# Kernel tuning notes

Hardware: AMD Instinct MI355X
Metric: run time of the kernel (lower is better)

## Reference

```python
import jax
import jax.numpy as jnp
import numpy as np

# Config mirroring GLOBAL_CONFIG['attn'] / kernel config in the source
BM = 64            # query-group (block) size; asserted 64 or 192 in source
TOP_KEYS = 0.1     # fraction of keys kept via top-k on colsum scores
MULTIPLE_OF = 64   # counts_multiple_of: indices_count rounded to this
LW1D = 0.15        # local_1d_window fraction
RAND_INV_PROB = 100

B, H, N, D = 1, 12, 2048, 128


def setup_inputs() -> dict:
    key = jax.random.key(0)
    kq, kk, kv, kc = jax.random.split(key, 4)
    shape = (B, H, N, D)
    q = jax.random.normal(kq, shape, dtype=jnp.float32)
    k = jax.random.normal(kk, shape, dtype=jnp.float32)
    v = jax.random.normal(kv, shape, dtype=jnp.float32)
    out_cache = jax.random.normal(kc, shape, dtype=jnp.float32)
    return {"q": q, "k": k, "v": v, "out_cache": out_cache}


def _static_1d_mask(n: int, bm: int, lw1d: float) -> jnp.ndarray:
    # initialize_1d_static_mask: per query-group local window centered at
    # qg*bm + bm//2, width int(lw1d*n), clipped to [0, n). Shape [qg, n].
    qg = n // bm
    ws = int(lw1d * n)
    centers = jnp.arange(qg) * bm + bm // 2          # [qg]
    j = jnp.arange(n)                                  # [n]
    lo = centers[:, None] - ws // 2
    hi = centers[:, None] + ws // 2
    return (j[None, :] >= lo) & (j[None, :] < hi)


def _scatter_true(mask, idx):
    # mask.scatter_(-1, idx, True) along last axis
    K = idx.shape[-1]
    n = mask.shape[-1]
    flat = mask.reshape(-1, n)
    fidx = idx.reshape(-1, K)
    rows = jnp.arange(flat.shape[0])[:, None]
    flat = flat.at[rows, fidx].set(True)
    return flat.reshape(mask.shape)


def _sparse_diff_attn(q, k, v, out_cache):
    b, h, n, d = q.shape
    qg = n // BM
    scale = 1.0 / jnp.sqrt(jnp.asarray(d, q.dtype))
    # dense scores (dense_colsum_attn computes these on the full step)
    scores = jnp.einsum('bhid,bhjd->bhij', q, k) * scale   # [b,h,n,n]
    probs = jax.nn.softmax(scores, axis=-1)
    # bs: column-sum of attention probabilities per query group  [b,h,qg,n]
    bs = probs.reshape(b, h, qg, BM, n).sum(axis=3)
    # indices_count = multiple_of * round(top_keys * n / multiple_of)
    indices_count = MULTIPLE_OF * int(round(TOP_KEYS * n / MULTIPLE_OF))
    rmask = jax.random.randint(jax.random.key(1), bs.shape, 0, RAND_INV_PROB) == 0
    _, idx = jax.lax.top_k(bs, indices_count)
    mask = _scatter_true(rmask, idx)                       # [b,h,qg,n]
    static = _static_1d_mask(n, BM, LW1D)                  # [qg,n]
    # video_query_groups: groups where static window + topk still sparse
    vqg = (static.sum(axis=-1, keepdims=True) + indices_count) < n  # [qg,1]
    mask = mask & vqg[None, None]
    mask = mask | static[None, None]
    # csp_attn: block-sparse attention; every query i in group i//BM attends
    # only to keys selected in mask[.., i//BM, :]
    full_mask = jnp.repeat(mask, BM, axis=2)               # [b,h,n,n]
    sp_scores = jnp.where(full_mask, scores, -jnp.inf)
    sp_probs = jax.nn.softmax(sp_scores, axis=-1)
    sp_out = jnp.einsum('bhij,bhjd->bhid', sp_probs, v)
    # sparse step: o = o_cache + csp_attn(...)  (sign = +1)
    return out_cache + sp_out


def reference(q, k, v, out_cache):
    return _sparse_diff_attn(q, k, v, out_cache)
```

## Files before the change

### kernel.cpp

```cpp
#include <hip/hip_runtime.h>
#include <math.h>

constexpr int Hh   = 12;
constexpr int Nn   = 2048;
constexpr int Dd   = 128;
constexpr int BMq  = 64;
constexpr int QGg  = 32;
constexpr int KSEL = 192;
constexpr int CK   = 32;
constexpr float SCALE = 0.08838834764831845f;

typedef _Float16 v8h __attribute__((ext_vector_type(8)));
typedef float    v4f __attribute__((ext_vector_type(4)));

__device__ __attribute__((aligned(16))) _Float16 g_qh[(size_t)Hh*Nn*Dd];
__device__ __attribute__((aligned(16))) _Float16 g_ql[(size_t)Hh*Nn*Dd];
__device__ __attribute__((aligned(16))) _Float16 g_kh[(size_t)Hh*Nn*Dd];
__device__ __attribute__((aligned(16))) _Float16 g_kl[(size_t)Hh*Nn*Dd];
__device__ float          g_lp[(size_t)Hh*Nn*16];
__device__ float          g_bs[(size_t)Hh*QGg*Nn];
__device__ unsigned short g_sel[Hh*QGg*Nn];
__device__ int            g_cnt[Hh*QGg];

__device__ __forceinline__ unsigned int rotl32(unsigned int x, int n){
  return (x << n) | (x >> (32 - n));
}

__device__ __forceinline__ unsigned pack2h(_Float16 a, _Float16 b){
  unsigned short ua, ub;
  __builtin_memcpy(&ua, &a, 2);
  __builtin_memcpy(&ub, &b, 2);
  return (unsigned)ua | ((unsigned)ub << 16);
}

__device__ __forceinline__ void tf2x32(unsigned int k0, unsigned int k1,
                                       unsigned int x0, unsigned int x1,
                                       unsigned int &o0, unsigned int &o1){
  const unsigned int ks2 = 0x1BD11BDAu ^ k0 ^ k1;
  x0 += k0; x1 += k1;
  x0 += x1; x1 = rotl32(x1,13); x1 ^= x0;
  x0 += x1; x1 = rotl32(x1,15); x1 ^= x0;
  x0 += x1; x1 = rotl32(x1,26); x1 ^= x0;
  x0 += x1; x1 = rotl32(x1, 6); x1 ^= x0;
  x0 += k1; x1 += ks2 + 1u;
  x0 += x1; x1 = rotl32(x1,17); x1 ^= x0;
  x0 += x1; x1 = rotl32(x1,29); x1 ^= x0;
  x0 += x1; x1 = rotl32(x1,16); x1 ^= x0;
  x0 += x1; x1 = rotl32(x1,24); x1 ^= x0;
  x0 += ks2; x1 += k0 + 2u;
  x0 += x1; x1 = rotl32(x1,13); x1 ^= x0;
  x0 += x1; x1 = rotl32(x1,15); x1 ^= x0;
  x0 += x1; x1 = rotl32(x1,26); x1 ^= x0;
  x0 += x1; x1 = rotl32(x1, 6); x1 ^= x0;
  x0 += k0; x1 += k1 + 3u;
  x0 += x1; x1 = rotl32(x1,17); x1 ^= x0;
  x0 += x1; x1 = rotl32(x1,29); x1 ^= x0;
  x0 += x1; x1 = rotl32(x1,16); x1 ^= x0;
  x0 += x1; x1 = rotl32(x1,24); x1 ^= x0;
  x0 += k1; x1 += ks2 + 4u;
  x0 += x1; x1 = rotl32(x1,13); x1 ^= x0;
  x0 += x1; x1 = rotl32(x1,15); x1 ^= x0;
  x0 += x1; x1 = rotl32(x1,26); x1 ^= x0;
  x0 += x1; x1 = rotl32(x1, 6); x1 ^= x0;
  x0 += ks2; x1 += k0 + 5u;
  o0 = x0; o1 = x1;
}

__device__ __forceinline__ bool jax_rand01(unsigned int idx,
                                           unsigned int k1a, unsigned int k1b,
                                           unsigned int k2a, unsigned int k2b){
  unsigned int h0, h1, l0, l1;
  tf2x32(k1a, k1b, 0u, idx, h0, h1);
  tf2x32(k2a, k2b, 0u, idx, l0, l1);
  unsigned int h = h0 ^ h1;
  unsigned int l = l0 ^ l1;
  unsigned int off = ((h % 100u) * 96u + (l % 100u)) % 100u;
  return off == 0u;
}

__global__ __launch_bounds__(256) void k0_cvt(const float* __restrict__ Q,
                                              const float* __restrict__ K){
  const int bid = blockIdx.x;
  const int t = threadIdx.x;
  const int kc = t >> 6, ln = t & 63;
  const int row = ln & 15;
  const int col = kc*32 + (ln >> 4)*8;
  const size_t src = ((size_t)bid*16 + row)*Dd + col;
  const size_t ob  = (((size_t)bid)*4 + kc)*512 + (size_t)ln*8;

  float4 qa = *(const float4*)(Q + src);
  float4 qb = *(const float4*)(Q + src + 4);
  float qs[8] = {qa.x*SCALE, qa.y*SCALE, qa.z*SCALE, qa.w*SCALE,
                 qb.x*SCALE, qb.y*SCALE, qb.z*SCALE, qb.w*SCALE};
  v8h qh, ql;
  #pragma unroll
  for (int j = 0; j < 8; ++j){
    _Float16 hi = (_Float16)qs[j];
    qh[j] = hi;
    ql[j] = (_Float16)(qs[j] - (float)hi);
  }
  *(v8h*)&g_qh[ob] = qh;
  *(v8h*)&g_ql[ob] = ql;

  float4 ka = *(const float4*)(K + src);
  float4 kb = *(const float4*)(K + src + 4);
  float ks[8] = {ka.x, ka.y, ka.z, ka.w, kb.x, kb.y, kb.z, kb.w};
  v8h kh, kl;
  #pragma unroll
  for (int j = 0; j < 8; ++j){
    _Float16 hi = (_Float16)ks[j];
    kh[j] = hi;
    kl[j] = (_Float16)(ks[j] - (float)hi);
  }
  *(v8h*)&g_kh[ob] = kh;
  *(v8h*)&g_kl[ob] = kl;
}

__global__ __launch_bounds__(256) void k1_rowsum(){
  const int bid0 = blockIdx.x;
  const int w = (bid0 & 7)*384 + (bid0 >> 3);
  const int jb = w & 15, gp = (w >> 4) & 15, h = w >> 8;
  const int t = threadIdx.x;
  const int wv = t >> 6, ln = t & 63;
  const int nidx = ln & 15, quad = ln >> 4;
  const size_t lnoff = (size_t)ln*8;
  const size_t habase = ((size_t)h*128 + gp*8 + wv*2)*4;
  const size_t hbbase = ((size_t)h*128 + jb*8)*4;

  v4f acc[2][8];
  #pragma unroll
  for (int tr = 0; tr < 2; ++tr)
    #pragma unroll
    for (int tc = 0; tc < 8; ++tc)
      acc[tr][tc] = (v4f){0.f, 0.f, 0.f, 0.f};

  for (int kc = 0; kc < 4; ++kc){
    v8h ahi[2], alo[2];
    #pragma unroll
    for (int tr = 0; tr < 2; ++tr){
      const size_t ab = (habase + tr*4 + kc)*512 + lnoff;
      ahi[tr] = *(const v8h*)&g_qh[ab];
      alo[tr] = *(const v8h*)&g_ql[ab];
    }
    v8h bhi[8], blo[8];
    #pragma unroll
    for (int tc = 0; tc < 8; ++tc){
      const size_t bb = (hbbase + tc*4 + kc)*512 + lnoff;
      bhi[tc] = *(const v8h*)&g_kh[bb];
      blo[tc] = *(const v8h*)&g_kl[bb];
    }
    #pragma unroll
    for (int tr = 0; tr < 2; ++tr)
      #pragma unroll
      for (int tc = 0; tc < 8; ++tc){
        acc[tr][tc] = __builtin_amdgcn_mfma_f32_16x16x32_f16(ahi[tr], bhi[tc], acc[tr][tc], 0, 0, 0);
        acc[tr][tc] = __builtin_amdgcn_mfma_f32_16x16x32_f16(ahi[tr], blo[tc], acc[tr][tc], 0, 0, 0);
        acc[tr][tc] = __builtin_amdgcn_mfma_f32_16x16x32_f16(alo[tr], bhi[tc], acc[tr][tc], 0, 0, 0);
      }
  }

  #pragma unroll
  for (int tr = 0; tr < 2; ++tr){
    float rs[4] = {0.f, 0.f, 0.f, 0.f};
    #pragma unroll
    for (int tc = 0; tc < 8; ++tc){
      #pragma unroll
      for (int r = 0; r < 4; ++r){
        rs[r] += __expf(acc[tr][tc][r]);
      }
    }
    #pragma unroll
    for (int r = 0; r < 4; ++r){
      float v = rs[r];
      v += __shfl_xor(v, 1);
      v += __shfl_xor(v, 2);
      v += __shfl_xor(v, 4);
      v += __shfl_xor(v, 8);
      rs[r] = v;
    }
    if (nidx == 0){
      #pragma unroll
      for (int r = 0; r < 4; ++r){
        const int row = (wv*2+tr)*16 + quad*4 + r;
        g_lp[((size_t)h*Nn + gp*128 + row)*16 + jb] = rs[r];
      }
    }
  }
}

__global__ __launch_bounds__(256) void k2r_colsum(){
  const int bid0 = blockIdx.x;
  const int w = (bid0 & 7)*384 + (bid0 >> 3);
  const int jb = w & 15, gp = (w >> 4) & 15, h = w >> 8;
  const int t = threadIdx.x;
  const int wv = t >> 6, ln = t & 63;
  const int nidx = ln & 15, quad = ln >> 4;
  const size_t lnoff = (size_t)ln*8;
  const size_t habase = ((size_t)h*128 + gp*8 + wv*2)*4;
  const size_t hbbase = ((size_t)h*128 + jb*8)*4;

  __shared__ float il_s[128];
  __shared__ float part[4][128];
  if (t < 128){
    const float* lp = &g_lp[((size_t)h*Nn + gp*128 + t)*16];
    float s = 0.f;
    #pragma unroll
    for (int x = 0; x < 16; ++x) s += lp[x];
    il_s[t] = 1.0f / s;
  }
  __syncthreads();

  v4f acc[2][8];
  #pragma unroll
  for (int tr = 0; tr < 2; ++tr)
    #pragma unroll
    for (int tc = 0; tc < 8; ++tc)
      acc[tr][tc] = (v4f){0.f, 0.f, 0.f, 0.f};

  for (int kc = 0; kc < 4; ++kc){
    v8h ahi[2], alo[2];
    #pragma unroll
    for (int tr = 0; tr < 2; ++tr){
      const size_t ab = (habase + tr*4 + kc)*512 + lnoff;
      ahi[tr] = *(const v8h*)&g_qh[ab];
      alo[tr] = *(const v8h*)&g_ql[ab];
    }
    v8h bhi[8], blo[8];
    #pragma unroll
    for (int tc = 0; tc < 8; ++tc){
      const size_t bb = (hbbase + tc*4 + kc)*512 + lnoff;
      bhi[tc] = *(const v8h*)&g_kh[bb];
      blo[tc] = *(const v8h*)&g_kl[bb];
    }
    #pragma unroll
    for (int tr = 0; tr < 2; ++tr)
      #pragma unroll
      for (int tc = 0; tc < 8; ++tc){
        acc[tr][tc] = __builtin_amdgcn_mfma_f32_16x16x32_f16(ahi[tr], bhi[tc], acc[tr][tc], 0, 0, 0);
        acc[tr][tc] = __builtin_amdgcn_mfma_f32_16x16x32_f16(ahi[tr], blo[tc], acc[tr][tc], 0, 0, 0);
        acc[tr][tc] = __builtin_amdgcn_mfma_f32_16x16x32_f16(alo[tr], bhi[tc], acc[tr][tc], 0, 0, 0);
      }
  }

  float csg[8];
  #pragma unroll
  for (int tc = 0; tc < 8; ++tc) csg[tc] = 0.f;
  #pragma unroll
  for (int tr = 0; tr < 2; ++tr){
    #pragma unroll
    for (int tc = 0; tc < 8; ++tc){
      float cs = 0.f;
      #pragma unroll
      for (int r = 0; r < 4; ++r){
        const int row = (wv*2+tr)*16 + quad*4 + r;
        cs += __expf(acc[tr][tc][r]) * il_s[row];
      }
      cs += __shfl_xor(cs, 16);
      cs += __shfl_xor(cs, 32);
      csg[tc] += cs;
    }
  }
  if (ln < 16){
    #pragma unroll
    for (int tc = 0; tc < 8; ++tc) part[wv][tc*16 + nidx] = csg[tc];
  }
  __syncthreads();
  const int col = t & 127, grp = t >> 7;
  g_bs[((size_t)h*QGg + gp*2 + grp)*Nn + jb*128 + col] =
      part[grp*2][col] + part[grp*2 + 1][col];
}

__global__ __launch_bounds__(256) void k2b_mask(){
  const int bid = blockIdx.x, g = bid % QGg, t = threadIdx.x;
  const int wv = t >> 6, lw = t & 63;
  __shared__ int hist[256];
  __shared__ int wsum[4];
  __shared__ int selb_s, selgt_s;
  __shared__ int csel;
  __shared__ int eqn;
  __shared__ int eqpos[Nn];
  const float* src = g_bs + (size_t)bid*Nn;
  float mine[8];
  {
    float4 a = *(const float4*)&src[t*4];
    float4 b = *(const float4*)&src[1024 + t*4];
    mine[0]=a.x; mine[1]=a.y; mine[2]=a.z; mine[3]=a.w;
    mine[4]=b.x; mine[5]=b.y; mine[6]=b.z; mine[7]=b.w;
  }
  if (t == 0){ csel = 0; eqn = 0; }
  unsigned int bu8[8];
  #pragma unroll
  for (int u = 0; u < 8; ++u) bu8[u] = __float_as_uint(mine[u]);

  unsigned int k1a, k1b, k2a, k2b;
  tf2x32(0u, 1u, 0u, 0u, k1a, k1b);
  tf2x32(0u, 1u, 0u, 1u, k2a, k2b);

  unsigned int pref = 0u;
  unsigned int msk  = 0u;
  int rem = KSEL;
  #pragma unroll
  for (int pass = 3; pass >= 0; --pass){
    const int shift = pass*8;
    hist[t] = 0;
    __syncthreads();
    #pragma unroll
    for (int u = 0; u < 8; ++u){
      if ((bu8[u] & msk) == pref)
        atomicAdd(&hist[(bu8[u] >> shift) & 0xFFu], 1);
    }
    __syncthreads();
    const int hcnt = hist[t];
    int s = hcnt;
    #pragma unroll
    for (int d = 1; d < 64; d <<= 1){
      int tmp = __shfl_down(s, d);
      if (lw + d < 64) s += tmp;
    }
    if (lw == 0) wsum[wv] = s;
    __syncthreads();
    int base = 0;
    #pragma unroll
    for (int w2 = 1; w2 < 4; ++w2) if (wv + w2 < 4) base += wsum[wv + w2];
    const int gt_incl = s + base;
    const int gt = gt_incl - hcnt;
    if (gt < rem && gt_incl >= rem){ selb_s = t; selgt_s = gt; }
    __syncthreads();
    pref |= ((unsigned)selb_s) << shift;
    msk  |= 0xFFu << shift;
    rem  -= selgt_s;
  }
  const unsigned int T = pref;
  const int need = rem;

  #pragma unroll
  for (int u = 0; u < 8; ++u){
    int j = (u < 4) ? (t*4 + u) : (1024 + t*4 + u - 4);
    if (bu8[u] == T){
      int s = atomicAdd(&eqn, 1);
      eqpos[s] = j;
    }
  }
  __syncthreads();
  const int en = eqn;

  const int lo = g*BMq + BMq/2 - 153;
  const int hi = g*BMq + BMq/2 + 153;
  const int ssum = ((hi < Nn) ? hi : Nn) - ((lo > 0) ? lo : 0);
  const bool vqg = (ssum + KSEL) < Nn;

  #pragma unroll
  for (int u = 0; u < 8; ++u){
    int j = (u < 4) ? (t*4 + u) : (1024 + t*4 + u - 4);
    unsigned int bu = bu8[u];
    bool topk = bu > T;
    if (!topk && bu == T){
      int tr = 0;
      for (int i = 0; i < en; ++i)
        tr += (eqpos[i] < j) ? 1 : 0;
      topk = (tr < need);
    }
    bool rnd = jax_rand01((unsigned)(bid*Nn + j), k1a, k1b, k2a, k2b);
    bool st  = (j >= lo) && (j < hi);
    bool selb = st || ((rnd || topk) && vqg);
    if (selb){
      int slot = atomicAdd(&csel, 1);
      g_sel[(size_t)bid*Nn + slot] = (unsigned short)j;
    }
  }
  __syncthreads();
  if (t == 0) g_cnt[bid] = csel;
}

__global__ __launch_bounds__(256) void k3_attn(const float* __restrict__ K,
                                               const float* __restrict__ V,
                                               const float* __restrict__ OC,
                                               float* __restrict__ out){
  const int bid0 = blockIdx.x;
  const int w    = (bid0 & 7)*96 + (bid0 >> 3);
  const int half = w & 1;
  const int gg   = w >> 1;
  const int h = gg / QGg, g = gg % QGg;
  const int t = threadIdx.x;
  const int wv = t >> 6, ln = t & 63;
  const int nidx = ln & 15, quad = ln >> 4;
  const int qtile = wv >> 1, kdt = wv & 1;

  __shared__ _Float16 kh_s[CK][136];
  __shared__ _Float16 kl_s[CK][136];
  __shared__ float    vT[Dd][33];
  __shared__ _Float16 p_h[32][40];
  __shared__ _Float16 p_l[32][40];
  __shared__ float    l_part[2][32];
  __shared__ float    l_s[32];

  const int c = g_cnt[gg];
  const unsigned short* sel = g_sel + (size_t)gg*Nn;

  const int rb = g*4 + half*2 + qtile;
  v8h aHi[4], aLo[4];
  #pragma unroll
  for (int kc = 0; kc < 4; ++kc){
    const size_t ab = (((size_t)h*128 + rb)*4 + kc)*512 + (size_t)ln*8;
    aHi[kc] = *(const v8h*)&g_qh[ab];
    aLo[kc] = *(const v8h*)&g_ql[ab];
  }

  if (t < 64) l_part[t >> 5][t & 31] = 0.0f;
  __syncthreads();

  v4f acc[4];
  #pragma unroll
  for (int dt = 0; dt < 4; ++dt) acc[dt] = (v4f){0.f, 0.f, 0.f, 0.f};

  for (int c0 = 0; c0 < c; c0 += CK){
    const int cc = ((c - c0) < CK) ? (c - c0) : CK;
    #pragma unroll
    for (int it = 0; it < 4; ++it){
      int e = it*256 + t, row = e >> 5, c4 = e & 31;
      int j = (row < cc) ? (int)sel[c0 + row] : 0;
      float4 kv = ((const float4*)(K + ((size_t)h*Nn + j)*Dd))[c4];
      float xs[4] = {kv.x, kv.y, kv.z, kv.w};
      _Float16 hh[4], ll[4];
      #pragma unroll
      for (int m = 0; m < 4; ++m){
        _Float16 hi = (_Float16)xs[m];
        hh[m] = hi;
        ll[m] = (_Float16)(xs[m] - (float)hi);
      }
      *(unsigned*)&kh_s[row][c4*4 + 0] = pack2h(hh[0], hh[1]);
      *(unsigned*)&kh_s[row][c4*4 + 2] = pack2h(hh[2], hh[3]);
      *(unsigned*)&kl_s[row][c4*4 + 0] = pack2h(ll[0], ll[1]);
      *(unsigned*)&kl_s[row][c4*4 + 2] = pack2h(ll[2], ll[3]);
    }
    #pragma unroll
    for (int it = 0; it < 4; ++it){
      int e = it*256 + t, row = e >> 5, c4 = e & 31;
      int j = (row < cc) ? (int)sel[c0 + row] : 0;
      float4 vv = ((const float4*)(V + ((size_t)h*Nn + j)*Dd))[c4];
      vT[c4*4+0][row] = vv.x;
      vT[c4*4+1][row] = vv.y;
      vT[c4*4+2][row] = vv.z;
      vT[c4*4+3][row] = vv.w;
    }
    __syncthreads();
    v4f sc = (v4f){0.f, 0.f, 0.f, 0.f};
    #pragma unroll
    for (int kc = 0; kc < 4; ++kc){
      v8h bh = *(const v8h*)&kh_s[kdt*16 + nidx][kc*32 + quad*8];
      v8h bl = *(const v8h*)&kl_s[kdt*16 + nidx][kc*32 + quad*8];
      sc = __builtin_amdgcn_mfma_f32_16x16x32_f16(aHi[kc], bh, sc, 0, 0, 0);
      sc = __builtin_amdgcn_mfma_f32_16x16x32_f16(aHi[kc], bl, sc, 0, 0, 0);
      sc = __builtin_amdgcn_mfma_f32_16x16x32_f16(aLo[kc], bh, sc, 0, 0, 0);
    }
    {
      const int k_loc = kdt*16 + nidx;
      float rs[4];
      #pragma unroll
      for (int r = 0; r < 4; ++r){
        float sv = (k_loc < cc) ? __expf(sc[r]) : 0.f;
        rs[r] = sv;
        _Float16 hi = (_Float16)sv;
        const int row = qtile*16 + quad*4 + r;
        p_h[row][k_loc] = hi;
        p_l[row][k_loc] = (_Float16)(sv - (float)hi);
      }
      #pragma unroll
      for (int r = 0; r < 4; ++r){
        float v = rs[r];
        v += __shfl_xor(v, 1);
        v += __shfl_xor(v, 2);
        v += __shfl_xor(v, 4);
        v += __shfl_xor(v, 8);
        rs[r] = v;
      }
      if (nidx == 0){
        #pragma unroll
        for (int r = 0; r < 4; ++r)
          l_part[kdt][qtile*16 + quad*4 + r] += rs[r];
      }
    }
    __syncthreads();
    {
      v8h ph = *(const v8h*)&p_h[qtile*16 + nidx][quad*8];
      v8h pl = *(const v8h*)&p_l[qtile*16 + nidx][quad*8];
      #pragma unroll
      for (int dt = 0; dt < 4; ++dt){
        const int d = (kdt*4 + dt)*16 + nidx;
        v8h vh, vl;
        #pragma unroll
        for (int jj = 0; jj < 8; ++jj){
          float vv = vT[d][quad*8 + jj];
          _Float16 hi = (_Float16)vv;
          vh[jj] = hi;
          vl[jj] = (_Float16)(vv - (float)hi);
        }
        acc[dt] = __builtin_amdgcn_mfma_f32_16x16x32_f16(ph, vh, acc[dt], 0, 0, 0);
        acc[dt] = __builtin_amdgcn_mfma_f32_16x16x32_f16(ph, vl, acc[dt], 0, 0, 0);
        acc[dt] = __builtin_amdgcn_mfma_f32_16x16x32_f16(pl, vh, acc[dt], 0, 0, 0);
      }
    }
    __syncthreads();
  }

  if (t < 32) l_s[t] = 1.0f / (l_part[0][t] + l_part[1][t]);
  __syncthreads();

  #pragma unroll
  for (int dt = 0; dt < 4; ++dt){
    const int d = (kdt*4 + dt)*16 + nidx;
    #pragma unroll
    for (int r = 0; r < 4; ++r){
      const int row = qtile*16 + quad*4 + r;
      const float il = l_s[row];
      const size_t o = ((size_t)h*Nn + (size_t)g*BMq + half*32 + row)*Dd + d;
      out[o] = acc[dt][r]*il + OC[o];
    }
  }
}

extern "C" void kernel_launch(void* const* d_in, const int* in_sizes, int n_in,
                              void* d_out, int out_size, void* d_ws, size_t ws_size,
                              hipStream_t stream) {
  (void)in_sizes; (void)n_in; (void)out_size; (void)d_ws; (void)ws_size;
  const float* Q  = (const float*)d_in[0];
  const float* K  = (const float*)d_in[1];
  const float* V  = (const float*)d_in[2];
  const float* OC = (const float*)d_in[3];
  float* out = (float*)d_out;
  hipLaunchKernelGGL(k0_cvt,     dim3(Hh*128),   dim3(256), 0, stream, Q, K);
  hipLaunchKernelGGL(k1_rowsum,  dim3(Hh*16*16), dim3(256), 0, stream);
  hipLaunchKernelGGL(k2r_colsum, dim3(Hh*16*16), dim3(256), 0, stream);
  hipLaunchKernelGGL(k2b_mask,   dim3(Hh*QGg),   dim3(256), 0, stream);
  hipLaunchKernelGGL(k3_attn,    dim3(Hh*QGg*2), dim3(256), 0, stream, K, V, OC, out);
}
```

Measured before the change: 272.4 us.

## Prefetch next K/V chunk into registers and store V pre-split as swizzled fp16

Gathered K and V rows for the next chunk are loaded into registers right after the shared-memory barrier, so the global-memory latency of the next chunk overlaps the MFMA work on the current one. V is split into hi/lo fp16 once at shared-memory store time, using a XOR-swizzled transposed layout. This lets the PV stage read 8-wide vectors directly instead of doing scalar float reads plus conversions. The cost is higher register pressure from holding eight float4 values, which may reduce occupancy.

```diff
diff --git a/kernel.cpp b/kernel.cpp
--- a/kernel.cpp
+++ b/kernel.cpp
@@ -388,7 +388,8 @@
 
   __shared__ _Float16 kh_s[CK][136];
   __shared__ _Float16 kl_s[CK][136];
-  __shared__ float    vT[Dd][33];
+  __shared__ _Float16 vTh[Dd][40];
+  __shared__ _Float16 vTl[Dd][40];
   __shared__ _Float16 p_h[32][40];
   __shared__ _Float16 p_l[32][40];
   __shared__ float    l_part[2][32];
@@ -407,19 +408,31 @@
   }
 
   if (t < 64) l_part[t >> 5][t & 31] = 0.0f;
-  __syncthreads();
+
+  float4 kreg[4], vreg[4];
+  {
+    const int cc0 = (c < CK) ? c : CK;
+    #pragma unroll
+    for (int it = 0; it < 4; ++it){
+      int e = it*256 + t, row = e >> 5, c4 = e & 31;
+      int j = (row < cc0) ? (int)sel[row] : 0;
+      kreg[it] = ((const float4*)(K + ((size_t)h*Nn + j)*Dd))[c4];
+      vreg[it] = ((const float4*)(V + ((size_t)h*Nn + j)*Dd))[c4];
+    }
+  }
 
   v4f acc[4];
   #pragma unroll
   for (int dt = 0; dt < 4; ++dt) acc[dt] = (v4f){0.f, 0.f, 0.f, 0.f};
+
+  const int cg = (quad ^ ((nidx >> 2) & 3)) * 8;
 
   for (int c0 = 0; c0 < c; c0 += CK){
     const int cc = ((c - c0) < CK) ? (c - c0) : CK;
     #pragma unroll
     for (int it = 0; it < 4; ++it){
       int e = it*256 + t, row = e >> 5, c4 = e & 31;
-      int j = (row < cc) ? (int)sel[c0 + row] : 0;
-      float4 kv = ((const float4*)(K + ((size_t)h*Nn + j)*Dd))[c4];
+      float4 kv = kreg[it];
       float xs[4] = {kv.x, kv.y, kv.z, kv.w};
       _Float16 hh[4], ll[4];
       #pragma unroll
@@ -432,18 +445,30 @@
       *(unsigned*)&kh_s[row][c4*4 + 2] = pack2h(hh[2], hh[3]);
       *(unsigned*)&kl_s[row][c4*4 + 0] = pack2h(ll[0], ll[1]);
       *(unsigned*)&kl_s[row][c4*4 + 2] = pack2h(ll[2], ll[3]);
-    }
-    #pragma unroll
-    for (int it = 0; it < 4; ++it){
-      int e = it*256 + t, row = e >> 5, c4 = e & 31;
-      int j = (row < cc) ? (int)sel[c0 + row] : 0;
-      float4 vv = ((const float4*)(V + ((size_t)h*Nn + j)*Dd))[c4];
-      vT[c4*4+0][row] = vv.x;
-      vT[c4*4+1][row] = vv.y;
-      vT[c4*4+2][row] = vv.z;
-      vT[c4*4+3][row] = vv.w;
-    }
-    __syncthreads();
+      float4 vv = vreg[it];
+      float vs[4] = {vv.x, vv.y, vv.z, vv.w};
+      const int swz = row ^ ((c4 & 3) << 3);
+      #pragma unroll
+      for (int m = 0; m < 4; ++m){
+        _Float16 hi = (_Float16)vs[m];
+        vTh[c4*4 + m][swz] = hi;
+        vTl[c4*4 + m][swz] = (_Float16)(vs[m] - (float)hi);
+      }
+    }
+    __syncthreads();
+    {
+      const int nc0 = c0 + CK;
+      if (nc0 < c){
+        const int ncc = ((c - nc0) < CK) ? (c - nc0) : CK;
+        #pragma unroll
+        for (int it = 0; it < 4; ++it){
+          int e = it*256 + t, row = e >> 5, c4 = e & 31;
+          int j = (row < ncc) ? (int)sel[nc0 + row] : 0;
+          kreg[it] = ((const float4*)(K + ((size_t)h*Nn + j)*Dd))[c4];
+          vreg[it] = ((const float4*)(V + ((size_t)h*Nn + j)*Dd))[c4];
+        }
+      }
+    }
     v4f sc = (v4f){0.f, 0.f, 0.f, 0.f};
     #pragma unroll
     for (int kc = 0; kc < 4; ++kc){
@@ -487,14 +512,8 @@
       #pragma unroll
       for (int dt = 0; dt < 4; ++dt){
         const int d = (kdt*4 + dt)*16 + nidx;
-        v8h vh, vl;
-        #pragma unroll
-        for (int jj = 0; jj < 8; ++jj){
-          float vv = vT[d][quad*8 + jj];
-          _Float16 hi = (_Float16)vv;
-          vh[jj] = hi;
-          vl[jj] = (_Float16)(vv - (float)hi);
-        }
+        v8h vh = *(const v8h*)&vTh[d][cg];
+        v8h vl = *(const v8h*)&vTl[d][cg];
         acc[dt] = __builtin_amdgcn_mfma_f32_16x16x32_f16(ph, vh, acc[dt], 0, 0, 0);
         acc[dt] = __builtin_amdgcn_mfma_f32_16x16x32_f16(ph, vl, acc[dt], 0, 0, 0);
         acc[dt] = __builtin_amdgcn_mfma_f32_16x16x32_f16(pl, vh, acc[dt], 0, 0, 0);
```

Result: no change. 270.0 us (-0.9%).
